# Optimization experiments

Hardware: AMD Instinct MI355X
Metric: run time of the kernel (lower is better)

The kernel has to match this reference:

```python
import jax, jax.numpy as jnp
import numpy as np

L, Q, H, B = 200, 21, 128, 256
LQ = L * Q


def _dca_mask():
    # Faithful to the original code: loop bounds use l_alphabet (q), not seq_len.
    m = np.zeros((LQ, LQ), np.float32)
    for i in range(Q):
        for j in range(i):
            m[i * Q:(i + 1) * Q, j * Q:(j + 1) * Q] = 1.0
    return jnp.asarray(m)


def _row_mask():
    # row_mask[l, d] = 1 if d < (l+1)*q : valid prefix rows for FFNet i=l+1
    return jnp.asarray((np.arange(LQ)[None, :] < (np.arange(1, L) * Q)[:, None]).astype(np.float32))


def setup_inputs() -> dict:
    key = jax.random.key(0)
    ks = jax.random.split(key, 12)
    # one-hot encoded sequences (B, L, Q)
    idx = jax.random.randint(ks[0], (B, L), 0, Q)
    x = jax.nn.one_hot(idx, Q, dtype=jnp.float32)
    row_mask = _row_mask()  # (L-1, LQ)
    W1 = 0.02 * jax.random.normal(ks[1], (L - 1, LQ, H), dtype=jnp.float32) * row_mask[:, :, None]
    return {
        "x": x,
        "DCA_bias": jnp.zeros((LQ,), jnp.float32),
        "DCA_weights": 0.01 * jax.random.normal(ks[2], (LQ, LQ), dtype=jnp.float32),
        "w0": 0.1 * jax.random.normal(ks[3], (Q,), dtype=jnp.float32),   # nn_bias0 weight (q,1) collapsed
        "b0": 0.1 * jax.random.normal(ks[4], (Q,), dtype=jnp.float32),
        "W1": W1,
        "b1": 0.02 * jax.random.normal(ks[5], (L - 1, H), dtype=jnp.float32),
        "W2": 0.08 * jax.random.normal(ks[6], (L - 1, H, H), dtype=jnp.float32),
        "b2": 0.02 * jax.random.normal(ks[7], (L - 1, H), dtype=jnp.float32),
        "Wout": 0.08 * jax.random.normal(ks[8], (L - 1, H, Q), dtype=jnp.float32),
        "bout": 0.02 * jax.random.normal(ks[9], (L - 1, Q), dtype=jnp.float32),
    }


def _lrelu(v):
    return jnp.where(v >= 0, v, 0.1 * v)  # negative_slope=0.1


def reference(x, DCA_bias, DCA_weights, w0, b0, W1, b1, W2, b2, Wout, bout):
    x_flat = x.reshape(x.shape[0], LQ)
    # arDCA: masked dense matmul
    logits_dca = (DCA_bias + x_flat @ (DCA_weights * _dca_mask())).reshape(-1, L, Q)
    # arNN position 0: Linear(1, q) applied to ones -> w0 + b0 broadcast over batch
    out0 = jnp.broadcast_to(w0 + b0, (x.shape[0], Q))
    # positions 1..L-1: ragged FFNets batched as padded stacked GEMMs.
    # Padded weight rows are masked to zero so x_flat @ W1_eff[l] == prefix_l @ W1_l.
    W1_eff = W1 * _row_mask()[:, :, None]          # (L-1, LQ, H)
    h1 = _lrelu(jnp.einsum('bd,ldh->blh', x_flat, W1_eff) + b1)   # (B, L-1, H)
    h2 = _lrelu(jnp.einsum('blh,lhk->blk', h1, W2) + b2)          # (B, L-1, H)
    out_rest = jnp.einsum('blh,lhq->blq', h2, Wout) + bout        # (B, L-1, Q)
    logits_nn = jnp.concatenate([out0[:, None, :], out_rest], axis=1)
    return logits_dca + logits_nn
```

## Files before the change

kernel.cpp:

```cpp
#include <hip/hip_runtime.h>


#define Lc   200
#define Qc   21
#define Hc   128
#define Bc   256
#define LQc  4200
#define LM1c 199
#define CH   48
#define NCH  5

__device__ __forceinline__ unsigned int bf16rne(float f) {
    unsigned int u = __float_as_uint(f);
    return u + 0x7fffu + ((u >> 16) & 1u);
}

__global__ __launch_bounds__(256) void k_idx(const float* __restrict__ x,
                                             unsigned char* __restrict__ idxT) {
    const int l = blockIdx.x;
    const int b = threadIdx.x;
    const float* p = x + ((size_t)b * Lc + l) * Qc;
    int id = 0;
#pragma unroll
    for (int c = 0; c < Qc; ++c) id = (p[c] > 0.5f) ? c : id;
    idxT[l * Bc + b] = (unsigned char)id;
}

__global__ __launch_bounds__(256) void k_dca(const float* __restrict__ DW,
                                             const float* __restrict__ bias,
                                             const float* __restrict__ w0,
                                             const float* __restrict__ b0,
                                             const unsigned char* __restrict__ idxT,
                                             float* __restrict__ out) {
    const int b = blockIdx.x / 5, chunk = blockIdx.x % 5;
    const int j0 = chunk * 1024 + threadIdx.x * 4;
    if (j0 >= LQc) return;
    float a[4];
    const float4 bv = *(const float4*)(bias + j0);
    a[0] = bv.x; a[1] = bv.y; a[2] = bv.z; a[3] = bv.w;
    if (j0 < Qc) {
#pragma unroll
        for (int e = 0; e < 4; ++e) {
            int j = j0 + e;
            if (j < Qc) a[e] += w0[j] + b0[j];
        }
    }
    if (j0 < (Qc - 1) * Qc) {
        const int lmin = j0 / Qc + 1;
        for (int l = lmin; l < Qc; ++l) {
            const int iv = idxT[l * Bc + b];
            const float4 v = *(const float4*)(DW + (size_t)(l * Qc + iv) * LQc + j0);
            const int thr = l * Qc;
            a[0] += (j0     < thr) ? v.x : 0.f;
            a[1] += (j0 + 1 < thr) ? v.y : 0.f;
            a[2] += (j0 + 2 < thr) ? v.z : 0.f;
            a[3] += (j0 + 3 < thr) ? v.w : 0.f;
        }
    }
    float4 o = {a[0], a[1], a[2], a[3]};
    *(float4*)(out + (size_t)b * LQc + j0) = o;
}

__global__ __launch_bounds__(1024, 2) void k_h1(const float* __restrict__ W1,
                                                const unsigned char* __restrict__ idxT,
                                                unsigned int* __restrict__ part) {
    const int bid = blockIdx.x;
    const int l = 198 - bid / NCH, c = bid % NCH;
    const int lo = c * CH;
    if (lo > l) return;
    const int hi = (l < lo + CH - 1) ? l : lo + CH - 1;
    const int n = hi - lo + 1;

    const int t = threadIdx.x;
    const int hq = t & 31;
    const int bg = t >> 5;

    __shared__ __align__(16) float tile[2][Qc * 132];
    __shared__ __align__(16) unsigned char idxs8[CH * Bc];

    {
        const int4* isrc = (const int4*)(idxT + lo * Bc);
        int4* idst = (int4*)idxs8;
        if (t < n * 16) idst[t] = isrc[t];
    }

    const float* Wsrc = W1 + (size_t)l * (LQc * Hc) + (size_t)lo * (Qc * Hc);
    if (t < 672) {
        const float4 q = ((const float4*)Wsrc)[t];
        *(float4*)&tile[0][(t >> 5) * 132 + (t & 31) * 4] = q;
    }
    __syncthreads();

    float4 acc[8];
#pragma unroll
    for (int j = 0; j < 8; ++j) acc[j] = (float4){0.f, 0.f, 0.f, 0.f};

    int cur = 0;
    for (int k = 0; k < n; ++k) {
        float4 p;
        const bool st = (k + 1 < n) && (t < 672);
        if (st) p = ((const float4*)(Wsrc + (size_t)(k + 1) * (Qc * Hc)))[t];
        const unsigned int* ibw = (const unsigned int*)&idxs8[k * Bc + bg * 8];
        const unsigned int u0 = ibw[0], u1 = ibw[1];
        const float* tb = &tile[cur][hq * 4];
#define ACC(j, u, sh) { \
        const float4 v = *(const float4*)(tb + (int)((u >> sh) & 0xffu) * 132); \
        acc[j].x += v.x; acc[j].y += v.y; acc[j].z += v.z; acc[j].w += v.w; }
        ACC(0, u0, 0) ACC(1, u0, 8) ACC(2, u0, 16) ACC(3, u0, 24)
        ACC(4, u1, 0) ACC(5, u1, 8) ACC(6, u1, 16) ACC(7, u1, 24)
#undef ACC
        if (st) *(float4*)&tile[cur ^ 1][(t >> 5) * 132 + (t & 31) * 4] = p;
        __syncthreads();
        cur ^= 1;
    }

    unsigned int* pb = part + ((size_t)(l * NCH + c) * Bc + bg * 8) * (Hc / 2) + hq * 2;
#pragma unroll
    for (int j = 0; j < 8; ++j) {
        const unsigned int d0 = (bf16rne(acc[j].x) >> 16) | (bf16rne(acc[j].y) & 0xffff0000u);
        const unsigned int d1 = (bf16rne(acc[j].z) >> 16) | (bf16rne(acc[j].w) & 0xffff0000u);
        *(uint2*)(pb + (size_t)j * (Hc / 2)) = make_uint2(d0, d1);
    }
}

__global__ __launch_bounds__(512, 4) void k_h2(const unsigned int* __restrict__ part,
                                               const float* __restrict__ W2,
                                               const float* __restrict__ b1,
                                               const float* __restrict__ b2,
                                               const float* __restrict__ Wout,
                                               const float* __restrict__ bout,
                                               float* __restrict__ out) {
    const int d = blockIdx.x;
    const int g = d >> 4, r = d & 7, half = (d >> 3) & 1;
    const int l = g * 8 + r;
    if (l >= LM1c) return;
    const int bbase = half * 128;
    const int t = threadIdx.x;
    const int tx = t & 15, ty = t >> 4;
    __shared__ float As[16][132];
    __shared__ float Bs[16][Hc];
    __shared__ float Ts[32][132];
    __shared__ float wl[Hc][24];
    float acc[4][8];
#pragma unroll
    for (int i = 0; i < 4; ++i)
#pragma unroll
        for (int j = 0; j < 8; ++j) acc[i][j] = 0.f;
    {
        const float* wsrc = Wout + (size_t)l * Hc * Qc;
        for (int i = t; i < Hc * Qc; i += 512) wl[i / Qc][i % Qc] = wsrc[i];
        if (t < Hc) { wl[t][21] = 0.f; wl[t][22] = 0.f; wl[t][23] = 0.f; }
    }
    const int skk = t >> 5, sms = (t & 31) * 4;
    const int am = t >> 2, akq = (t & 3) * 4;
    const int nch = l / CH + 1;
    const unsigned int* pl = part + ((size_t)(l * NCH) * Bc + bbase + am) * (Hc / 2);
    const float* W2l = W2 + (size_t)l * Hc * Hc;
    for (int ks = 0; ks < 8; ++ks) {
        const int kcu = ks * 8 + (t & 3) * 2;
        float4 a0 = {0.f, 0.f, 0.f, 0.f};
        for (int cc = 0; cc < nch; ++cc) {
            const uint2 w = *(const uint2*)(pl + (size_t)cc * Bc * (Hc / 2) + kcu);
            a0.x += __uint_as_float(w.x << 16);
            a0.y += __uint_as_float(w.x & 0xffff0000u);
            a0.z += __uint_as_float(w.y << 16);
            a0.w += __uint_as_float(w.y & 0xffff0000u);
        }
        const float4 bb = *(const float4*)(b1 + l * Hc + ks * 16 + akq);
        a0.x += bb.x; a0.y += bb.y; a0.z += bb.z; a0.w += bb.w;
        a0.x = (a0.x >= 0.f) ? a0.x : 0.1f * a0.x;
        a0.y = (a0.y >= 0.f) ? a0.y : 0.1f * a0.y;
        a0.z = (a0.z >= 0.f) ? a0.z : 0.1f * a0.z;
        a0.w = (a0.w >= 0.f) ? a0.w : 0.1f * a0.w;
        const int kb = ks * 16 + skk;
        *(float4*)&Bs[skk][sms] = *(const float4*)(W2l + (size_t)kb * Hc + sms);
        As[akq + 0][am] = a0.x; As[akq + 1][am] = a0.y;
        As[akq + 2][am] = a0.z; As[akq + 3][am] = a0.w;
        __syncthreads();
#pragma unroll
        for (int k = 0; k < 16; ++k) {
            float avr[4], bvr[8];
            *(float4*)&avr[0] = *(const float4*)&As[k][ty * 4];
            *(float4*)&bvr[0] = *(const float4*)&Bs[k][tx * 8];
            *(float4*)&bvr[4] = *(const float4*)&Bs[k][tx * 8 + 4];
#pragma unroll
            for (int i = 0; i < 4; ++i)
#pragma unroll
                for (int j = 0; j < 8; ++j) acc[i][j] += avr[i] * bvr[j];
        }
        __syncthreads();
    }
    float bz[8];
    *(float4*)&bz[0] = *(const float4*)(b2 + l * Hc + tx * 8);
    *(float4*)&bz[4] = *(const float4*)(b2 + l * Hc + tx * 8 + 4);
    float res[4][8];
#pragma unroll
    for (int i = 0; i < 4; ++i)
#pragma unroll
        for (int j = 0; j < 8; ++j) {
            float v = acc[i][j] + bz[j];
            res[i][j] = (v >= 0.f) ? v : 0.1f * v;
        }
    const int m = t & 127, qh = t >> 7;
    const int q0 = qh * 6;
    float racc[6];
#pragma unroll
    for (int qi = 0; qi < 6; ++qi) racc[qi] = 0.f;
    for (int c = 0; c < 4; ++c) {
        if ((tx >> 2) == c) {
#pragma unroll
            for (int i = 0; i < 4; ++i)
#pragma unroll
                for (int j = 0; j < 8; ++j) Ts[(tx & 3) * 8 + j][ty * 4 + i] = res[i][j];
        }
        __syncthreads();
#pragma unroll 4
        for (int rr = 0; rr < 32; ++rr) {
            const float v = Ts[rr][m];
            const float* wr = &wl[c * 32 + rr][q0];
#pragma unroll
            for (int qi = 0; qi < 6; ++qi) racc[qi] += v * wr[qi];
        }
        __syncthreads();
    }
    const int b = bbase + m;
    float* op = out + ((size_t)b * Lc + (l + 1)) * Qc;
    const float* bo = bout + l * Qc;
#pragma unroll
    for (int qi = 0; qi < 6; ++qi) {
        const int qq = q0 + qi;
        if (qq < Qc) op[qq] += racc[qi] + bo[qq];
    }
}

extern "C" void kernel_launch(void* const* d_in, const int* in_sizes, int n_in,
                              void* d_out, int out_size, void* d_ws, size_t ws_size,
                              hipStream_t stream) {
    const float* x    = (const float*)d_in[0];
    const float* bias = (const float*)d_in[1];
    const float* DW   = (const float*)d_in[2];
    const float* w0   = (const float*)d_in[3];
    const float* b0   = (const float*)d_in[4];
    const float* W1   = (const float*)d_in[5];
    const float* b1   = (const float*)d_in[6];
    const float* W2   = (const float*)d_in[7];
    const float* b2   = (const float*)d_in[8];
    const float* Wout = (const float*)d_in[9];
    const float* bout = (const float*)d_in[10];
    float* out = (float*)d_out;

    unsigned char* idxT = (unsigned char*)d_ws;
    unsigned int*  part = (unsigned int*)((char*)d_ws + 204800);

    k_idx<<<Lc, 256, 0, stream>>>(x, idxT);
    k_dca<<<Bc * 5, 256, 0, stream>>>(DW, bias, w0, b0, idxT, out);
    k_h1<<<LM1c * NCH, 1024, 0, stream>>>(W1, idxT, part);
    k_h2<<<400, 512, 0, stream>>>(part, W2, b1, b2, Wout, bout, out);
}
```

Before: 163.5 us.

## Restrict DCA kernel to nonzero first 441 columns and reorder after NN kernel

The DCA contribution is nonzero only for the first 20 positions (441 columns), so the DCA kernel now launches one block per batch row covering just those columns. The NN kernel writes its outputs directly, with bout and the DCA bias folded in, so it no longer has to read the output and add to it. The DCA kernel runs last and accumulates into the already-written output, writing bias, w0 and b0 for position 0. This removes the full-width DCA pass over all 4200 columns per sample, at the cost of a kernel ordering dependency.

```diff
diff --git a/kernel.cpp b/kernel.cpp
--- a/kernel.cpp
+++ b/kernel.cpp
@@ -26,39 +26,26 @@
     idxT[l * Bc + b] = (unsigned char)id;
 }
 
-__global__ __launch_bounds__(256) void k_dca(const float* __restrict__ DW,
+__global__ __launch_bounds__(512) void k_dca(const float* __restrict__ DW,
                                              const float* __restrict__ bias,
                                              const float* __restrict__ w0,
                                              const float* __restrict__ b0,
                                              const unsigned char* __restrict__ idxT,
                                              float* __restrict__ out) {
-    const int b = blockIdx.x / 5, chunk = blockIdx.x % 5;
-    const int j0 = chunk * 1024 + threadIdx.x * 4;
-    if (j0 >= LQc) return;
-    float a[4];
-    const float4 bv = *(const float4*)(bias + j0);
-    a[0] = bv.x; a[1] = bv.y; a[2] = bv.z; a[3] = bv.w;
-    if (j0 < Qc) {
-#pragma unroll
-        for (int e = 0; e < 4; ++e) {
-            int j = j0 + e;
-            if (j < Qc) a[e] += w0[j] + b0[j];
-        }
-    }
-    if (j0 < (Qc - 1) * Qc) {
-        const int lmin = j0 / Qc + 1;
-        for (int l = lmin; l < Qc; ++l) {
-            const int iv = idxT[l * Bc + b];
-            const float4 v = *(const float4*)(DW + (size_t)(l * Qc + iv) * LQc + j0);
-            const int thr = l * Qc;
-            a[0] += (j0     < thr) ? v.x : 0.f;
-            a[1] += (j0 + 1 < thr) ? v.y : 0.f;
-            a[2] += (j0 + 2 < thr) ? v.z : 0.f;
-            a[3] += (j0 + 3 < thr) ? v.w : 0.f;
-        }
-    }
-    float4 o = {a[0], a[1], a[2], a[3]};
-    *(float4*)(out + (size_t)b * LQc + j0) = o;
+    const int b = blockIdx.x;
+    const int t = threadIdx.x;
+    __shared__ int sidx[20];
+    if (t < 20) sidx[t] = idxT[(t + 1) * Bc + b];
+    __syncthreads();
+    if (t >= 441) return;
+    const int pos = t / 21, q = t - pos * 21;
+    const int j = t;
+    float acc = 0.f;
+    for (int lr = pos + 1; lr <= 20; ++lr)
+        acc += DW[(size_t)(lr * Qc + sidx[lr - 1]) * LQc + j];
+    float* op = out + (size_t)b * LQc;
+    if (pos == 0) op[j] = acc + bias[j] + w0[q] + b0[q];
+    else          op[j] += acc;
 }
 
 __global__ __launch_bounds__(1024, 2) void k_h1(const float* __restrict__ W1,
@@ -129,6 +116,7 @@
                                                const float* __restrict__ b2,
                                                const float* __restrict__ Wout,
                                                const float* __restrict__ bout,
+                                               const float* __restrict__ bias,
                                                float* __restrict__ out) {
     const int d = blockIdx.x;
     const int g = d >> 4, r = d & 7, half = (d >> 3) & 1;
@@ -141,6 +129,7 @@
     __shared__ float Bs[16][Hc];
     __shared__ float Ts[32][132];
     __shared__ float wl[Hc][24];
+    __shared__ float blsh[24];
     float acc[4][8];
 #pragma unroll
     for (int i = 0; i < 4; ++i)
@@ -150,6 +139,8 @@
         const float* wsrc = Wout + (size_t)l * Hc * Qc;
         for (int i = t; i < Hc * Qc; i += 512) wl[i / Qc][i % Qc] = wsrc[i];
         if (t < Hc) { wl[t][21] = 0.f; wl[t][22] = 0.f; wl[t][23] = 0.f; }
+        if (t < Qc) blsh[t] = bout[l * Qc + t] + bias[(l + 1) * Qc + t];
+        else if (t < 24) blsh[t] = 0.f;
     }
     const int skk = t >> 5, sms = (t & 31) * 4;
     const int am = t >> 2, akq = (t & 3) * 4;
@@ -225,11 +216,10 @@
     }
     const int b = bbase + m;
     float* op = out + ((size_t)b * Lc + (l + 1)) * Qc;
-    const float* bo = bout + l * Qc;
 #pragma unroll
     for (int qi = 0; qi < 6; ++qi) {
         const int qq = q0 + qi;
-        if (qq < Qc) op[qq] += racc[qi] + bo[qq];
+        if (qq < Qc) op[qq] = racc[qi] + blsh[qq];
     }
 }
 
@@ -253,7 +243,7 @@
     unsigned int*  part = (unsigned int*)((char*)d_ws + 204800);
 
     k_idx<<<Lc, 256, 0, stream>>>(x, idxT);
-    k_dca<<<Bc * 5, 256, 0, stream>>>(DW, bias, w0, b0, idxT, out);
     k_h1<<<LM1c * NCH, 1024, 0, stream>>>(W1, idxT, part);
-    k_h2<<<400, 512, 0, stream>>>(part, W2, b1, b2, Wout, bout, out);
-}
+    k_h2<<<400, 512, 0, stream>>>(part, W2, b1, b2, Wout, bout, bias, out);
+    k_dca<<<Bc, 512, 0, stream>>>(DW, bias, w0, b0, idxT, out);
+}
```

Measured after the change: 156.7 us. -4.2%, faster.
